# Performance work log

Hardware: AMD Instinct MI355X
Metric: run time of the kernel (lower is better)

The kernel has to match this reference:

```python
import jax, jax.numpy as jnp
import numpy as np

# Static problem configuration
NUM_GRAPHS = 64
NODES_PER_GRAPH = 2048          # divisible by OUT_H
NODE_EMB_DIM = 256              # divisible by OUT_W
COND_EMB_DIM = 64
OUT_H, OUT_W = 16, 8            # AdaptiveAvgPool2d output -> pooled dim H*W = 128
MLP_H = 256
BN_EPS = 1e-5


def setup_inputs() -> dict:
    key = jax.random.key(0)
    ks = jax.random.split(key, 8)
    N = NUM_GRAPHS * NODES_PER_GRAPH
    x = jax.random.normal(ks[0], (N, NODE_EMB_DIM), dtype=jnp.float32)
    # equal contiguous segments: node i belongs to graph i // NODES_PER_GRAPH
    batch = jnp.repeat(jnp.arange(NUM_GRAPHS, dtype=jnp.int64), NODES_PER_GRAPH)
    conditioner_z_ref = jax.random.normal(ks[1], (N, COND_EMB_DIM), dtype=jnp.float32)
    mlp_in = COND_EMB_DIM + OUT_H * OUT_W
    W1 = jax.random.normal(ks[2], (mlp_in, MLP_H), dtype=jnp.float32) / np.sqrt(mlp_in)
    b1 = jnp.zeros((MLP_H,), dtype=jnp.float32)
    gamma = jnp.ones((MLP_H,), dtype=jnp.float32)
    beta = jnp.zeros((MLP_H,), dtype=jnp.float32)
    W2 = jax.random.normal(ks[3], (MLP_H, 3), dtype=jnp.float32) / np.sqrt(MLP_H)
    b2 = jnp.zeros((3,), dtype=jnp.float32)
    return {"x": x, "batch": batch, "conditioner_z_ref": conditioner_z_ref,
            "W1": W1, "b1": b1, "gamma": gamma, "beta": beta, "W2": W2, "b2": b2}


def _adaptive_pool(x):
    # x: [N_total, D] with equal contiguous segments of NODES_PER_GRAPH rows per graph.
    # AdaptiveAvgPool2d((OUT_H, OUT_W)) on each [n, D] "image"; since n % OUT_H == 0
    # and D % OUT_W == 0 the adaptive bins are uniform -> exact reshape-mean.
    B = x.shape[0] // NODES_PER_GRAPH
    xg = x.reshape(B, OUT_H, NODES_PER_GRAPH // OUT_H, OUT_W, NODE_EMB_DIM // OUT_W)
    pooled = xg.mean(axis=(2, 4))                 # [B, OUT_H, OUT_W]
    return pooled.reshape(B, OUT_H * OUT_W)       # [B, H*W]


def reference(x, batch, conditioner_z_ref, W1, b1, gamma, beta, W2, b2):
    batch_pooled = _adaptive_pool(x)                          # [B, H*W]
    gathered = batch_pooled[batch]                            # [N, H*W]
    h = jnp.concatenate([conditioner_z_ref, gathered], axis=1)  # [N, cond + H*W]
    # Linear -> BatchNorm1d (training-mode batch stats, biased var) -> GELU (exact)
    h = h @ W1 + b1                                           # [N, MLP_H]
    mean = h.mean(axis=0)
    var = h.var(axis=0)
    h = (h - mean) * jax.lax.rsqrt(var + BN_EPS) * gamma + beta
    h = jax.nn.gelu(h, approximate=False)
    return h @ W2 + b2                                        # [N, 3]
```

## Files before the change

kernel.cpp:

```cpp
#include <hip/hip_runtime.h>
#include <math.h>

#define NG    64
#define NPG   2048
#define NTOT  (NG*NPG)
#define ZD    64
#define PD    128
#define MH    256

typedef __attribute__((ext_vector_type(8))) short bf16x8;
typedef __attribute__((ext_vector_type(4))) float f32x4;

__device__ __forceinline__ unsigned short f2bf(float f){
  unsigned u = __float_as_uint(f);
  unsigned r = u + 0x7FFFu + ((u >> 16) & 1u);
  return (unsigned short)(r >> 16);
}
__device__ __forceinline__ float bf2f(unsigned short s){
  return __uint_as_float(((unsigned)s) << 16);
}
__device__ __forceinline__ float gelu_f(float x){
  float t = 0.7978845608028654f * fmaf(0.044715f * x, x * x, x);
  float e = __expf(2.0f * t);
  float th = 1.0f - 2.0f / (e + 1.0f);
  return 0.5f * x * (1.0f + th);
}

__launch_bounds__(256)
__global__ void k1_pool_zstat(const float* __restrict__ x, const float* __restrict__ z,
                              float* __restrict__ pooled, float* __restrict__ St,
                              float* __restrict__ C){
  __shared__ __align__(16) unsigned short s_zt[64 * 264];
  __shared__ float s_cred[4096];
  int tid = threadIdx.x;

  if (blockIdx.x >= 256){
    int bi = blockIdx.x - 256;
    int b  = bi >> 4;
    int oh = bi & 15;
    int c4 = tid & 63;
    int rq = tid >> 6;
    const float4* x4 = (const float4*)x;
    size_t base = (size_t)(b * NPG + oh * 128) * 64;
    float4 acc = make_float4(0.f, 0.f, 0.f, 0.f);
    #pragma unroll 8
    for (int i = 0; i < 32; i++){
      float4 v = x4[base + (size_t)(rq + i * 4) * 64 + c4];
      acc.x += v.x; acc.y += v.y; acc.z += v.z; acc.w += v.w;
    }
    s_cred[tid] = acc.x + acc.y + acc.z + acc.w;
    __syncthreads();
    if (tid < 8){
      float s = 0.f;
      #pragma unroll
      for (int w = 0; w < 4; w++)
        #pragma unroll
        for (int j = 0; j < 8; j++)
          s += s_cred[w * 64 + tid * 8 + j];
      pooled[b * PD + oh * 8 + tid] = s * (1.0f / 4096.0f);
    }
    return;
  }

  int blk = blockIdx.x;
  int g = blk >> 2, q4 = blk & 3;
  int lane = tid & 63, wave = tid >> 6;
  int col = lane & 15, quad = lane >> 4;
  const float4* z4 = (const float4*)z + ((size_t)g * 2048 + q4 * 512) * 16;
  int d4 = tid & 15;

  f32x4 acc[4][4];
  #pragma unroll
  for (int a = 0; a < 4; a++)
    #pragma unroll
    for (int b = 0; b < 4; b++) acc[a][b] = (f32x4)(0.f);
  float s0 = 0.f, s1 = 0.f, s2 = 0.f, s3 = 0.f;

  for (int ch = 0; ch < 2; ch++){
    #pragma unroll
    for (int i = 0; i < 16; i++){
      int idx = tid + i * 256;
      int m = idx >> 4;
      float4 v = z4[ch * 4096 + idx];
      s0 += v.x; s1 += v.y; s2 += v.z; s3 += v.w;
      s_zt[(d4 * 4 + 0) * 264 + m] = f2bf(v.x);
      s_zt[(d4 * 4 + 1) * 264 + m] = f2bf(v.y);
      s_zt[(d4 * 4 + 2) * 264 + m] = f2bf(v.z);
      s_zt[(d4 * 4 + 3) * 264 + m] = f2bf(v.w);
    }
    __syncthreads();
    #pragma unroll
    for (int ks = 0; ks < 2; ks++){
      int k0 = wave * 64 + ks * 32;
      bf16x8 fr[4];
      #pragma unroll
      for (int t = 0; t < 4; t++)
        fr[t] = *(const bf16x8*)&s_zt[(t * 16 + col) * 264 + k0 + quad * 8];
      #pragma unroll
      for (int mt = 0; mt < 4; mt++)
        #pragma unroll
        for (int nt = 0; nt < 4; nt++)
          acc[mt][nt] = __builtin_amdgcn_mfma_f32_16x16x32_bf16(fr[mt], fr[nt], acc[mt][nt], 0, 0, 0);
    }
    __syncthreads();
  }

  s0 += __shfl_xor(s0, 16); s0 += __shfl_xor(s0, 32);
  s1 += __shfl_xor(s1, 16); s1 += __shfl_xor(s1, 32);
  s2 += __shfl_xor(s2, 16); s2 += __shfl_xor(s2, 32);
  s3 += __shfl_xor(s3, 16); s3 += __shfl_xor(s3, 32);
  if (quad == 0){
    atomicAdd(&St[(d4 * 4 + 0) * 64 + g], s0);
    atomicAdd(&St[(d4 * 4 + 1) * 64 + g], s1);
    atomicAdd(&St[(d4 * 4 + 2) * 64 + g], s2);
    atomicAdd(&St[(d4 * 4 + 3) * 64 + g], s3);
  }

  #pragma unroll
  for (int w = 0; w < 4; w++){
    if (wave == w){
      #pragma unroll
      for (int mt = 0; mt < 4; mt++)
        #pragma unroll
        for (int nt = 0; nt < 4; nt++)
          #pragma unroll
          for (int r = 0; r < 4; r++){
            int p = mt * 16 + quad * 4 + r;
            int qc = nt * 16 + col;
            if (w == 0) s_cred[p * 64 + qc]  = acc[mt][nt][r];
            else        s_cred[p * 64 + qc] += acc[mt][nt][r];
          }
    }
    __syncthreads();
  }
  for (int f = tid; f < 4096; f += 256)
    atomicAdd(&C[f], s_cred[f]);
}

__launch_bounds__(256)
__global__ void k2_stats(const float* __restrict__ pooled, const float* __restrict__ W1,
                         const float* __restrict__ b1, const float* __restrict__ gamma,
                         const float* __restrict__ beta, const float* __restrict__ C,
                         const float* __restrict__ St, float* __restrict__ Aj,
                         float* __restrict__ cprime, unsigned short* __restrict__ Wbf){
  __shared__ float pl[64 * 129];
  int tid = threadIdx.x;
  int jc = tid >> 6, lane = tid & 63;
  int j = blockIdx.x * 4 + jc;

  Wbf[(size_t)j * 64 + lane] = f2bf(W1[(size_t)lane * 256 + j]);

  for (int idx = tid; idx < 8192; idx += 256)
    pl[(idx >> 7) * 129 + (idx & 127)] = pooled[idx];
  __syncthreads();

  float g = b1[j];
  #pragma unroll 8
  for (int k = 0; k < 128; k++)
    g = fmaf(pl[lane * 129 + k], W1[(size_t)(ZD + k) * MH + j], g);

  float wl = W1[(size_t)lane * MH + j];
  float t1 = 0.f, t2 = 0.f;
  #pragma unroll
  for (int q = 0; q < 64; q++){
    float wq = __uint_as_float(__builtin_amdgcn_readlane(__float_as_uint(wl), q));
    t1 = fmaf(C [q * 64 + lane], wq, t1);
    t2 = fmaf(St[q * 64 + lane], wq, t2);
  }
  float v_wcw = wl * t1;
  float v_gs  = g * t2;
  float v_s   = t2;
  float v_g   = g;
  float v_g2  = g * g;
  #pragma unroll
  for (int off = 32; off; off >>= 1){
    v_wcw += __shfl_xor(v_wcw, off);
    v_gs  += __shfl_xor(v_gs , off);
    v_s   += __shfl_xor(v_s  , off);
    v_g   += __shfl_xor(v_g  , off);
    v_g2  += __shfl_xor(v_g2 , off);
  }
  const float invN = 1.0f / (float)NTOT;
  float mean = v_s * invN + v_g * (1.0f / 64.0f);
  float eh2  = v_wcw * invN + 2.0f * invN * v_gs + v_g2 * (1.0f / 64.0f);
  float var  = eh2 - mean * mean;
  float aj = gamma[j] * rsqrtf(var + 1e-5f);
  if (lane == 0) Aj[j] = aj;
  cprime[lane * MH + j] = fmaf(aj, g, beta[j] - aj * mean);
}

__launch_bounds__(256, 2)
__global__ void final_kernel(const float* __restrict__ z, const unsigned short* __restrict__ Wbf,
                             const float* __restrict__ Aj, const float* __restrict__ cp,
                             const float* __restrict__ W2, const float* __restrict__ b2,
                             float* __restrict__ out){
  __shared__ __align__(16) unsigned short zt[128 * 136];
  __shared__ float slab[2][384];
  int tid = threadIdx.x;
  int n0 = blockIdx.x * 128;
  int g = blockIdx.x >> 4;

  const float4* z4 = (const float4*)z + (size_t)n0 * 16;
  #pragma unroll
  for (int i = 0; i < 8; i++){
    int idx = tid + i * 256;
    int m = idx >> 4, d4 = idx & 15;
    float4 v = z4[idx];
    ushort4 h, l;
    h.x = f2bf(v.x); l.x = f2bf(v.x - bf2f(h.x));
    h.y = f2bf(v.y); l.y = f2bf(v.y - bf2f(h.y));
    h.z = f2bf(v.z); l.z = f2bf(v.z - bf2f(h.z));
    h.w = f2bf(v.w); l.w = f2bf(v.w - bf2f(h.w));
    *(ushort4*)&zt[m * 136 + d4 * 4]      = h;
    *(ushort4*)&zt[m * 136 + 64 + d4 * 4] = l;
  }
  __syncthreads();

  int lane = tid & 63, wave = tid >> 6;
  int wm = wave & 1, wn = wave >> 1;
  int col = lane & 15, quad = lane >> 4;
  int mbase = wm * 64, nbase = wn * 128;

  f32x4 acc[4][8];
  #pragma unroll
  for (int mt = 0; mt < 4; mt++)
    #pragma unroll
    for (int nt = 0; nt < 8; nt++) acc[mt][nt] = (f32x4)(0.f);

  #pragma unroll
  for (int ks = 0; ks < 4; ks++){
    int k0 = ks * 32;
    bf16x8 af[4];
    #pragma unroll
    for (int mt = 0; mt < 4; mt++)
      af[mt] = *(const bf16x8*)&zt[(mbase + mt * 16 + col) * 136 + k0 + quad * 8];
    #pragma unroll
    for (int nt = 0; nt < 8; nt++){
      bf16x8 bv = *(const bf16x8*)&Wbf[(size_t)(nbase + nt * 16 + col) * 64 + (ks & 1) * 32 + quad * 8];
      #pragma unroll
      for (int mt = 0; mt < 4; mt++)
        acc[mt][nt] = __builtin_amdgcn_mfma_f32_16x16x32_bf16(af[mt], bv, acc[mt][nt], 0, 0, 0);
    }
  }

  float aj[8], cj[8], w2a[8], w2b[8], w2c[8];
  #pragma unroll
  for (int nt = 0; nt < 8; nt++){
    int j = nbase + nt * 16 + col;
    aj[nt] = Aj[j];
    cj[nt] = cp[g * MH + j];
    w2a[nt] = W2[j * 3 + 0];
    w2b[nt] = W2[j * 3 + 1];
    w2c[nt] = W2[j * 3 + 2];
  }

  #pragma unroll
  for (int mt = 0; mt < 4; mt++){
    #pragma unroll
    for (int r = 0; r < 4; r++){
      float o0 = 0.f, o1 = 0.f, o2 = 0.f;
      #pragma unroll
      for (int nt = 0; nt < 8; nt++){
        float h  = fmaf(aj[nt], acc[mt][nt][r], cj[nt]);
        float ge = gelu_f(h);
        o0 = fmaf(ge, w2a[nt], o0);
        o1 = fmaf(ge, w2b[nt], o1);
        o2 = fmaf(ge, w2c[nt], o2);
      }
      #pragma unroll
      for (int off = 8; off; off >>= 1){
        o0 += __shfl_xor(o0, off);
        o1 += __shfl_xor(o1, off);
        o2 += __shfl_xor(o2, off);
      }
      if (col == 0){
        int node = mbase + mt * 16 + quad * 4 + r;
        slab[wn][node * 3 + 0] = o0;
        slab[wn][node * 3 + 1] = o1;
        slab[wn][node * 3 + 2] = o2;
      }
    }
  }
  __syncthreads();
  float b2v[3] = {b2[0], b2[1], b2[2]};
  for (int f = tid; f < 384; f += 256)
    out[(size_t)blockIdx.x * 384 + f] = slab[0][f] + slab[1][f] + b2v[f % 3];
}

extern "C" void kernel_launch(void* const* d_in, const int* in_sizes, int n_in,
                              void* d_out, int out_size, void* d_ws, size_t ws_size,
                              hipStream_t stream){
  (void)in_sizes; (void)n_in; (void)out_size; (void)ws_size;
  const float* x     = (const float*)d_in[0];
  const float* z     = (const float*)d_in[2];
  const float* W1    = (const float*)d_in[3];
  const float* b1    = (const float*)d_in[4];
  const float* gamma = (const float*)d_in[5];
  const float* beta  = (const float*)d_in[6];
  const float* W2    = (const float*)d_in[7];
  const float* b2    = (const float*)d_in[8];
  float* out = (float*)d_out;

  float* W = (float*)d_ws;
  float* pooled = W;
  float* St     = W + 8192;
  float* C      = W + 12288;
  float* Aj     = W + 16384;
  float* CP     = W + 16640;
  unsigned short* Wbf = (unsigned short*)(W + 33024);

  hipMemsetAsync((char*)d_ws + 8192 * 4, 0, 8192 * 4, stream);

  k1_pool_zstat<<<dim3(1280), dim3(256), 0, stream>>>(x, z, pooled, St, C);
  k2_stats     <<<dim3(64),   dim3(256), 0, stream>>>(pooled, W1, b1, gamma, beta, C, St, Aj, CP, Wbf);
  final_kernel <<<dim3(NTOT / 128), dim3(256), 0, stream>>>(z, Wbf, Aj, CP, W2, b2, out);
}
```

Before: 282.5 us.

## Use one z-stat block per graph and load z fragments directly in final GEMM

The z statistics stage now uses one block per graph instead of four. That block loops over all 2048 rows and writes per-graph column sums through a shared-memory reduction, so the St atomics and the memset of St are no longer needed. The final kernel drops its LDS staging of z and loads each MFMA A-fragment straight from global memory, splitting it into bf16 hi/lo parts in registers. This removes LDS traffic and a sync, but it uses fewer blocks in k1 (64 graph blocks) and relies on uncoalesced, strided global loads in the final kernel.

```diff
diff --git a/kernel.cpp b/kernel.cpp
--- a/kernel.cpp
+++ b/kernel.cpp
@@ -32,10 +32,11 @@
                               float* __restrict__ C){
   __shared__ __align__(16) unsigned short s_zt[64 * 264];
   __shared__ float s_cred[4096];
+  __shared__ float s_st[4][64];
   int tid = threadIdx.x;
 
-  if (blockIdx.x >= 256){
-    int bi = blockIdx.x - 256;
+  if (blockIdx.x >= 64){
+    int bi = blockIdx.x - 64;
     int b  = bi >> 4;
     int oh = bi & 15;
     int c4 = tid & 63;
@@ -62,11 +63,10 @@
     return;
   }
 
-  int blk = blockIdx.x;
-  int g = blk >> 2, q4 = blk & 3;
+  int g = blockIdx.x;
   int lane = tid & 63, wave = tid >> 6;
   int col = lane & 15, quad = lane >> 4;
-  const float4* z4 = (const float4*)z + ((size_t)g * 2048 + q4 * 512) * 16;
+  const float4* z4 = (const float4*)z + (size_t)g * 2048 * 16;
   int d4 = tid & 15;
 
   f32x4 acc[4][4];
@@ -76,7 +76,7 @@
     for (int b = 0; b < 4; b++) acc[a][b] = (f32x4)(0.f);
   float s0 = 0.f, s1 = 0.f, s2 = 0.f, s3 = 0.f;
 
-  for (int ch = 0; ch < 2; ch++){
+  for (int ch = 0; ch < 8; ch++){
     #pragma unroll
     for (int i = 0; i < 16; i++){
       int idx = tid + i * 256;
@@ -109,12 +109,11 @@
   s1 += __shfl_xor(s1, 16); s1 += __shfl_xor(s1, 32);
   s2 += __shfl_xor(s2, 16); s2 += __shfl_xor(s2, 32);
   s3 += __shfl_xor(s3, 16); s3 += __shfl_xor(s3, 32);
-  if (quad == 0){
-    atomicAdd(&St[(d4 * 4 + 0) * 64 + g], s0);
-    atomicAdd(&St[(d4 * 4 + 1) * 64 + g], s1);
-    atomicAdd(&St[(d4 * 4 + 2) * 64 + g], s2);
-    atomicAdd(&St[(d4 * 4 + 3) * 64 + g], s3);
-  }
+  if (quad == 0)
+    *(float4*)&s_st[wave][d4 * 4] = make_float4(s0, s1, s2, s3);
+  __syncthreads();
+  if (tid < 64)
+    St[tid * 64 + g] = s_st[0][tid] + s_st[1][tid] + s_st[2][tid] + s_st[3][tid];
 
   #pragma unroll
   for (int w = 0; w < 4; w++){
@@ -194,28 +193,11 @@
                              const float* __restrict__ Aj, const float* __restrict__ cp,
                              const float* __restrict__ W2, const float* __restrict__ b2,
                              float* __restrict__ out){
-  __shared__ __align__(16) unsigned short zt[128 * 136];
   __shared__ float slab[2][384];
   int tid = threadIdx.x;
   int n0 = blockIdx.x * 128;
   int g = blockIdx.x >> 4;
 
-  const float4* z4 = (const float4*)z + (size_t)n0 * 16;
-  #pragma unroll
-  for (int i = 0; i < 8; i++){
-    int idx = tid + i * 256;
-    int m = idx >> 4, d4 = idx & 15;
-    float4 v = z4[idx];
-    ushort4 h, l;
-    h.x = f2bf(v.x); l.x = f2bf(v.x - bf2f(h.x));
-    h.y = f2bf(v.y); l.y = f2bf(v.y - bf2f(h.y));
-    h.z = f2bf(v.z); l.z = f2bf(v.z - bf2f(h.z));
-    h.w = f2bf(v.w); l.w = f2bf(v.w - bf2f(h.w));
-    *(ushort4*)&zt[m * 136 + d4 * 4]      = h;
-    *(ushort4*)&zt[m * 136 + 64 + d4 * 4] = l;
-  }
-  __syncthreads();
-
   int lane = tid & 63, wave = tid >> 6;
   int wm = wave & 1, wn = wave >> 1;
   int col = lane & 15, quad = lane >> 4;
@@ -228,19 +210,35 @@
     for (int nt = 0; nt < 8; nt++) acc[mt][nt] = (f32x4)(0.f);
 
   #pragma unroll
-  for (int ks = 0; ks < 4; ks++){
-    int k0 = ks * 32;
-    bf16x8 af[4];
-    #pragma unroll
-    for (int mt = 0; mt < 4; mt++)
-      af[mt] = *(const bf16x8*)&zt[(mbase + mt * 16 + col) * 136 + k0 + quad * 8];
-    #pragma unroll
-    for (int nt = 0; nt < 8; nt++){
-      bf16x8 bv = *(const bf16x8*)&Wbf[(size_t)(nbase + nt * 16 + col) * 64 + (ks & 1) * 32 + quad * 8];
+  for (int kh = 0; kh < 2; kh++){
+    bf16x8 ah[4], al[4];
+    #pragma unroll
+    for (int mt = 0; mt < 4; mt++){
+      const float4* zr = (const float4*)(z + (size_t)(n0 + mbase + mt * 16 + col) * 64
+                                           + kh * 32 + quad * 8);
+      float4 v0 = zr[0], v1 = zr[1];
+      float f[8] = {v0.x, v0.y, v0.z, v0.w, v1.x, v1.y, v1.z, v1.w};
+      #pragma unroll
+      for (int e = 0; e < 8; e++){
+        unsigned short h = f2bf(f[e]);
+        ah[mt][e] = (short)h;
+        al[mt][e] = (short)f2bf(f[e] - bf2f(h));
+      }
+    }
+    bf16x8 bv[8];
+    #pragma unroll
+    for (int nt = 0; nt < 8; nt++)
+      bv[nt] = *(const bf16x8*)&Wbf[(size_t)(nbase + nt * 16 + col) * 64 + kh * 32 + quad * 8];
+    #pragma unroll
+    for (int nt = 0; nt < 8; nt++)
       #pragma unroll
       for (int mt = 0; mt < 4; mt++)
-        acc[mt][nt] = __builtin_amdgcn_mfma_f32_16x16x32_bf16(af[mt], bv, acc[mt][nt], 0, 0, 0);
-    }
+        acc[mt][nt] = __builtin_amdgcn_mfma_f32_16x16x32_bf16(ah[mt], bv[nt], acc[mt][nt], 0, 0, 0);
+    #pragma unroll
+    for (int nt = 0; nt < 8; nt++)
+      #pragma unroll
+      for (int mt = 0; mt < 4; mt++)
+        acc[mt][nt] = __builtin_amdgcn_mfma_f32_16x16x32_bf16(al[mt], bv[nt], acc[mt][nt], 0, 0, 0);
   }
 
   float aj[8], cj[8], w2a[8], w2b[8], w2c[8];
@@ -309,9 +307,9 @@
   float* CP     = W + 16640;
   unsigned short* Wbf = (unsigned short*)(W + 33024);
 
-  hipMemsetAsync((char*)d_ws + 8192 * 4, 0, 8192 * 4, stream);
-
-  k1_pool_zstat<<<dim3(1280), dim3(256), 0, stream>>>(x, z, pooled, St, C);
+  hipMemsetAsync((char*)d_ws + 12288 * 4, 0, 4096 * 4, stream);
+
+  k1_pool_zstat<<<dim3(1088), dim3(256), 0, stream>>>(x, z, pooled, St, C);
   k2_stats     <<<dim3(64),   dim3(256), 0, stream>>>(pooled, W1, b1, gamma, beta, C, St, Aj, CP, Wbf);
   final_kernel <<<dim3(NTOT / 128), dim3(256), 0, stream>>>(z, Wbf, Aj, CP, W2, b2, out);
 }
```

After: 331.8 us. +17.5%, slower.
